# Kernel tuning notes

Hardware: AMD Instinct MI355X
Metric: run time of the kernel (lower is better)

## Reference

```python
import jax, jax.numpy as jnp
import numpy as np

D_MODEL = 1024
NUM_HEADS = 16
D_K = D_MODEL // NUM_HEADS
SCALE = 1.0 / (D_K ** 0.5)


def setup_inputs() -> dict:
    key = jax.random.key(0)
    k1, k2, k3 = jax.random.split(key, 3)
    x = jax.random.normal(k1, (2, 2048, D_MODEL), dtype=jnp.float32)
    # torch nn.Linear weight layout: [out_features, in_features]; y = x @ W.T
    w_qkv = jax.random.normal(k2, (3 * D_MODEL, D_MODEL), dtype=jnp.float32) * (1.0 / np.sqrt(D_MODEL))
    w_out = jax.random.normal(k3, (D_MODEL, D_MODEL), dtype=jnp.float32) * (1.0 / np.sqrt(D_MODEL))
    return {"x": x, "w_qkv": w_qkv, "w_out": w_out}


def reference(x, w_qkv, w_out):
    b, s, _ = x.shape
    qkv = jnp.einsum("bsd,ed->bse", x, w_qkv)            # [b, s, 3*d_model]
    q, k, v = jnp.split(qkv, 3, axis=-1)
    # [b, s, h, d_k] -> [b, h, s, d_k]
    q = q.reshape(b, s, NUM_HEADS, D_K).transpose(0, 2, 1, 3)
    k = k.reshape(b, s, NUM_HEADS, D_K).transpose(0, 2, 1, 3)
    v = v.reshape(b, s, NUM_HEADS, D_K).transpose(0, 2, 1, 3)
    scores = jnp.einsum("bhqd,bhkd->bhqk", q, k) * SCALE   # [b, h, s, s]
    attn = jax.nn.softmax(scores, axis=-1)
    ctx = jnp.einsum("bhqk,bhkd->bhqd", attn, v)           # [b, h, s, d_k]
    ctx = ctx.transpose(0, 2, 1, 3).reshape(b, s, D_MODEL)
    return jnp.einsum("bsd,ed->bse", ctx, w_out)
```

## Files before the change

kernel.cpp:

```cpp
#include <hip/hip_runtime.h>

typedef __attribute__((ext_vector_type(8))) short bf16x8;
typedef __attribute__((ext_vector_type(4))) float f32x4;
typedef __attribute__((ext_vector_type(16))) float f32x16;
typedef __attribute__((ext_vector_type(4))) unsigned int u32x4;

#define MFMA16(A, B, C) __builtin_amdgcn_mfma_f32_16x16x32_bf16((A), (B), (C), 0, 0, 0)
#define MFMA32(A, B, C) __builtin_amdgcn_mfma_f32_32x32x16_bf16((A), (B), (C), 0, 0, 0)

static __device__ __forceinline__ unsigned short f32_to_bf16(float f) {
    unsigned int u = __builtin_bit_cast(unsigned int, f);
    u += 0x7fffu + ((u >> 16) & 1u);
    return (unsigned short)(u >> 16);
}

static __device__ __forceinline__ unsigned int cvtpk(float lo, float hi) {
    unsigned int r;
    asm("v_cvt_pk_bf16_f32 %0, %1, %2" : "=v"(r) : "v"(lo), "v"(hi));
    return r;
}

static __device__ __forceinline__ void gload16(const unsigned short* g, unsigned short* l) {
    __builtin_amdgcn_global_load_lds(
        (const __attribute__((address_space(1))) unsigned int*)g,
        (__attribute__((address_space(3))) unsigned int*)l, 16, 0, 0);
}

#define QSCALE 0.18033688011112042f

__global__ void cast3_f32_bf16(const float* __restrict__ x, const float* __restrict__ wq,
                               const float* __restrict__ wo,
                               unsigned short* __restrict__ xb, unsigned short* __restrict__ wqb,
                               unsigned short* __restrict__ wob) {
    int i = blockIdx.x * 256 + threadIdx.x;
    const float* src;
    unsigned short* dst;
    int off;
    if (i < 1048576)      { src = x;  dst = xb;  off = i; }
    else if (i < 1835008) { src = wq; dst = wqb; off = i - 1048576; }
    else                  { src = wo; dst = wob; off = i - 1835008; }
    float4 v = reinterpret_cast<const float4*>(src)[off];
    ushort4 o;
    o.x = f32_to_bf16(v.x);
    o.y = f32_to_bf16(v.y);
    o.z = f32_to_bf16(v.z);
    o.w = f32_to_bf16(v.w);
    reinterpret_cast<ushort4*>(dst)[off] = o;
}

template <int MODE, int BM, int BN, int WR, int WC>
__global__ __launch_bounds__(256, 2)
void gemm_bt(const unsigned short* __restrict__ Ag,
             const unsigned short* __restrict__ Bg,
             int N, int K,
             unsigned short* __restrict__ qO,
             unsigned short* __restrict__ kO,
             unsigned short* __restrict__ vO,
             float* __restrict__ fO)
{
    constexpr int BK = 64;
    constexpr int MFR = BM / WR / 16;
    constexpr int NFR = BN / WC / 16;
    __shared__ unsigned short SMEM[(BM + BN) * BK];
    unsigned short* sA = SMEM;
    unsigned short* sB = SMEM + BM * BK;

    const int m0 = blockIdx.y * BM;
    const int n0 = blockIdx.x * BN;
    const int t = threadIdx.x;
    const int lane = t & 63;
    const int wid = t >> 6;
    const int wr = wid / WC, wc = wid % WC;
    const int g = lane >> 4, r = lane & 15;
    const int lr8 = lane >> 3, lc = lane & 7;

    const f32x4 fzero = {0.f, 0.f, 0.f, 0.f};
    f32x4 acc[MFR][NFR];
#pragma unroll
    for (int mi = 0; mi < MFR; ++mi)
#pragma unroll
        for (int ni = 0; ni < NFR; ++ni) acc[mi][ni] = fzero;

    for (int k0 = 0; k0 < K; k0 += BK) {
        __syncthreads();
#pragma unroll
        for (int rep = 0; rep < BM / 32; ++rep) {
            const int rbase = rep * 32 + wid * 8;
            const int row = rbase + lr8;
            const int cs = lc ^ (row & 7);
            gload16(&Ag[(size_t)(m0 + row) * K + k0 + cs * 8], &sA[rbase * 64]);
        }
#pragma unroll
        for (int rep = 0; rep < BN / 32; ++rep) {
            const int rbase = rep * 32 + wid * 8;
            const int row = rbase + lr8;
            const int cs = lc ^ (row & 7);
            gload16(&Bg[(size_t)(n0 + row) * K + k0 + cs * 8], &sB[rbase * 64]);
        }
        __syncthreads();

#pragma unroll
        for (int ks = 0; ks < BK; ks += 32) {
            const int c = (ks >> 3) + g;
            bf16x8 af[MFR], bfr[NFR];
#pragma unroll
            for (int mi = 0; mi < MFR; ++mi) {
                const int row = wr * (BM / WR) + mi * 16 + r;
                af[mi] = *reinterpret_cast<const bf16x8*>(&sA[row * BK + ((c * 8) ^ ((row & 7) * 8))]);
            }
#pragma unroll
            for (int ni = 0; ni < NFR; ++ni) {
                const int row = wc * (BN / WC) + ni * 16 + r;
                bfr[ni] = *reinterpret_cast<const bf16x8*>(&sB[row * BK + ((c * 8) ^ ((row & 7) * 8))]);
            }
#pragma unroll
            for (int mi = 0; mi < MFR; ++mi)
#pragma unroll
                for (int ni = 0; ni < NFR; ++ni)
                    acc[mi][ni] = MFMA16(af[mi], bfr[ni], acc[mi][ni]);
        }
    }

    if (MODE == 0) {
        const int which = n0 >> 10;
        if (which == 2) {
#pragma unroll
            for (int mi = 0; mi < MFR; ++mi) {
#pragma unroll
                for (int ni = 0; ni < NFR; ++ni) {
                    const int mbase = m0 + wr * (BM / WR) + mi * 16 + 4 * g;
                    const int n = n0 + wc * (BN / WC) + ni * 16 + r;
                    const int b = mbase >> 11, s = mbase & 2047;
                    const int h = (n >> 6) & 15;
                    const int d = n & 63;
                    ushort4 v4;
                    v4.x = f32_to_bf16(acc[mi][ni][0]);
                    v4.y = f32_to_bf16(acc[mi][ni][1]);
                    v4.z = f32_to_bf16(acc[mi][ni][2]);
                    v4.w = f32_to_bf16(acc[mi][ni][3]);
                    *reinterpret_cast<ushort4*>(&vO[(((size_t)(b * 16 + h)) * 64 + d) * 2048 + s]) = v4;
                }
            }
        } else {
            __syncthreads();
            unsigned short* T = &SMEM[wid * 4096];
            const float scl = (which == 0) ? QSCALE : 1.0f;
#pragma unroll
            for (int mi = 0; mi < MFR; ++mi) {
#pragma unroll
                for (int ni = 0; ni < NFR; ++ni) {
#pragma unroll
                    for (int i = 0; i < 4; ++i) {
                        const int m_l = mi * 16 + 4 * g + i;
                        const int n_l = ni * 16 + r;
                        const int pos = m_l * 64 + ((((n_l >> 3) ^ (m_l & 7)) << 3) | (n_l & 7));
                        T[pos] = f32_to_bf16(acc[mi][ni][i] * scl);
                    }
                }
            }
            const int b = (m0 + wr * 64) >> 11;
            const int sbase = (m0 + wr * 64) & 2047;
            const int hh = ((n0 + wc * 64) >> 6) & 15;
            unsigned short* qk = (which == 0) ? qO : kO;
            const size_t base = (((size_t)(b * 16 + hh)) * 2048 + sbase) * 64;
#pragma unroll
            for (int it = 0; it < 8; ++it) {
                const int row = it * 8 + lr8;
                bf16x8 v8 = *reinterpret_cast<const bf16x8*>(&T[row * 64 + ((lc ^ (row & 7)) << 3)]);
                *reinterpret_cast<bf16x8*>(&qk[base + (size_t)row * 64 + lc * 8]) = v8;
            }
        }
    } else {
#pragma unroll
        for (int mi = 0; mi < MFR; ++mi) {
#pragma unroll
            for (int ni = 0; ni < NFR; ++ni) {
                const int mbase = m0 + wr * (BM / WR) + mi * 16 + 4 * g;
                const int n = n0 + wc * (BN / WC) + ni * 16 + r;
#pragma unroll
                for (int i = 0; i < 4; ++i)
                    fO[(size_t)(mbase + i) * N + n] = acc[mi][ni][i];
            }
        }
    }
}

__global__ __launch_bounds__(512, 4)
void attn_kernel(const unsigned short* __restrict__ Q,
                 const unsigned short* __restrict__ Kg,
                 const unsigned short* __restrict__ Vtg,
                 unsigned short* __restrict__ ctx)
{
    const int S = 2048;
    const int bid = blockIdx.x;
    const int swz = (bid & 7) * 64 + (bid >> 3);
    const int hb = swz >> 4;
    const int qb = swz & 15;
    const unsigned short* Qh = Q + (size_t)hb * S * 64;
    const unsigned short* Kh = Kg + (size_t)hb * S * 64;
    const unsigned short* Vh = Vtg + (size_t)hb * 64 * S;

    const int t = threadIdx.x, lane = t & 63, wid = t >> 6;
    const int half = wid >> 2, wq = wid & 3;
    const int l31 = lane & 31, lhi = lane >> 5;
    const int lr8 = lane >> 3, lc = lane & 7;
    const int q0 = qb * 128 + wq * 32;
    const int kbase = half * 1024;

    const int krow = (l31 & 19) | ((l31 & 4) << 1) | ((l31 & 8) >> 1);
    const int ksw = (krow & 7) ^ ((krow >> 3) & 3);
    const int vsw = (l31 & 7) ^ ((l31 >> 3) & 3);

    __shared__ unsigned short smem[2][2][2][64 * 64];

    bf16x8 qf[4];
#pragma unroll
    for (int dstep = 0; dstep < 4; ++dstep)
        qf[dstep] = *reinterpret_cast<const bf16x8*>(
            &Qh[(size_t)(q0 + l31) * 64 + dstep * 16 + lhi * 8]);

    f32x16 acc[2];
#pragma unroll
    for (int dt = 0; dt < 2; ++dt)
#pragma unroll
        for (int i = 0; i < 16; ++i) acc[dt][i] = 0.f;
    float lrun = 0.f;

#define STAGE(buf, k0)                                                                       \
    {                                                                                        \
        _Pragma("unroll")                                                                    \
        for (int rep = 0; rep < 2; ++rep) {                                                  \
            const int rbase = wq * 16 + rep * 8;                                             \
            const int row = rbase + lr8;                                                     \
            const int cs = lc ^ ((row & 7) ^ ((row >> 3) & 3));                              \
            gload16(&Kh[(size_t)((k0) + row) * 64 + cs * 8], &smem[half][buf][0][rbase * 64]); \
            gload16(&Vh[(size_t)row * S + (k0) + cs * 8], &smem[half][buf][1][rbase * 64]);  \
        }                                                                                    \
    }

    STAGE(0, kbase);

    for (int it = 0; it < 16; ++it) {
        __syncthreads();
        const int cur = it & 1;
        if (it < 15) {
            const int kn = kbase + (it + 1) * 64;
            if (cur) STAGE(0, kn) else STAGE(1, kn);
        }
        const unsigned short* kb = smem[half][cur][0];
        const unsigned short* vb = smem[half][cur][1];

        f32x16 st0, st1;
#pragma unroll
        for (int i = 0; i < 16; ++i) { st0[i] = 0.f; st1[i] = 0.f; }
        __builtin_amdgcn_s_setprio(1);
#pragma unroll
        for (int dstep = 0; dstep < 4; ++dstep) {
            const int c = dstep * 2 + lhi;
            bf16x8 kf0 = *reinterpret_cast<const bf16x8*>(&kb[krow * 64 + ((c ^ ksw) * 8)]);
            bf16x8 kf1 = *reinterpret_cast<const bf16x8*>(&kb[(32 + krow) * 64 + ((c ^ ksw) * 8)]);
            st0 = MFMA32(kf0, qf[dstep], st0);
            st1 = MFMA32(kf1, qf[dstep], st1);
        }
        __builtin_amdgcn_s_setprio(0);

#pragma unroll
        for (int i = 0; i < 16; ++i) {
            st0[i] = __builtin_amdgcn_exp2f(st0[i]);
            st1[i] = __builtin_amdgcn_exp2f(st1[i]);
        }
        float s8[8];
#pragma unroll
        for (int j = 0; j < 8; ++j)
            s8[j] = (st0[j] + st0[j + 8]) + (st1[j] + st1[j + 8]);
        lrun += ((s8[0] + s8[1]) + (s8[2] + s8[3])) + ((s8[4] + s8[5]) + (s8[6] + s8[7]));

        bf16x8 pf[4];
#define PACK8(stv, base, out)                                                  \
        {                                                                      \
            u32x4 wv;                                                          \
            wv[0] = cvtpk(stv[(base) + 0], stv[(base) + 1]);                   \
            wv[1] = cvtpk(stv[(base) + 2], stv[(base) + 3]);                   \
            wv[2] = cvtpk(stv[(base) + 4], stv[(base) + 5]);                   \
            wv[3] = cvtpk(stv[(base) + 6], stv[(base) + 7]);                   \
            out = __builtin_bit_cast(bf16x8, wv);                              \
        }
        PACK8(st0, 0, pf[0])
        PACK8(st0, 8, pf[1])
        PACK8(st1, 0, pf[2])
        PACK8(st1, 8, pf[3])
#undef PACK8

        __builtin_amdgcn_s_setprio(1);
#pragma unroll
        for (int dt = 0; dt < 2; ++dt) {
            const int rowd = dt * 32 + l31;
#pragma unroll
            for (int ks = 0; ks < 4; ++ks) {
                const int c = ks * 2 + lhi;
                bf16x8 vf = *reinterpret_cast<const bf16x8*>(&vb[rowd * 64 + ((c ^ vsw) * 8)]);
                acc[dt] = MFMA32(vf, pf[ks], acc[dt]);
            }
        }
        __builtin_amdgcn_s_setprio(0);
    }
#undef STAGE

    lrun += __shfl_xor(lrun, 32);

    __syncthreads();
    float* cb = reinterpret_cast<float*>(&smem[0][0][0][0]);
    if (half == 1) {
        float* base = cb + wq * 2112;
#pragma unroll
        for (int dt = 0; dt < 2; ++dt)
#pragma unroll
            for (int i = 0; i < 16; ++i)
                base[(dt * 16 + i) * 64 + lane] = acc[dt][i];
        if (lhi == 0) base[2048 + l31] = lrun;
    }
    __syncthreads();
    if (half == 0) {
        float* base = cb + wq * 2112;
        const float l1 = base[2048 + l31];
        const float rl = __builtin_amdgcn_rcpf(lrun + l1);
        const int b = hb >> 4, hh = hb & 15;
        const size_t rowbase = ((size_t)(b * 2048 + q0 + l31)) * 1024 + hh * 64;
#pragma unroll
        for (int dt = 0; dt < 2; ++dt) {
#pragma unroll
            for (int rg = 0; rg < 4; ++rg) {
                float v0 = (acc[dt][4 * rg + 0] + base[(dt * 16 + 4 * rg + 0) * 64 + lane]) * rl;
                float v1 = (acc[dt][4 * rg + 1] + base[(dt * 16 + 4 * rg + 1) * 64 + lane]) * rl;
                float v2 = (acc[dt][4 * rg + 2] + base[(dt * 16 + 4 * rg + 2) * 64 + lane]) * rl;
                float v3 = (acc[dt][4 * rg + 3] + base[(dt * 16 + 4 * rg + 3) * 64 + lane]) * rl;
                uint2 o;
                o.x = cvtpk(v0, v1);
                o.y = cvtpk(v2, v3);
                const int dbase = dt * 32 + rg * 8 + lhi * 4;
                *reinterpret_cast<uint2*>(&ctx[rowbase + dbase]) = o;
            }
        }
    }
}

extern "C" void kernel_launch(void* const* d_in, const int* in_sizes, int n_in,
                              void* d_out, int out_size, void* d_ws, size_t ws_size,
                              hipStream_t stream) {
    const float* x     = (const float*)d_in[0];
    const float* w_qkv = (const float*)d_in[1];
    const float* w_out = (const float*)d_in[2];
    float* out = (float*)d_out;

    unsigned short* xb    = (unsigned short*)d_ws;
    unsigned short* wqkvb = xb + 4194304;
    unsigned short* woutb = wqkvb + 3145728;
    unsigned short* qB    = woutb + 1048576;
    unsigned short* kB    = qB + 4194304;
    unsigned short* vB    = kB + 4194304;
    unsigned short* ctxB  = vB + 4194304;

    cast3_f32_bf16<<<8192, 256, 0, stream>>>(x, w_qkv, w_out, xb, wqkvb, woutb);

    gemm_bt<0, 128, 128, 2, 2><<<dim3(24, 32), 256, 0, stream>>>(xb, wqkvb, 3072, 1024, qB, kB, vB, nullptr);

    attn_kernel<<<512, 512, 0, stream>>>(qB, kB, vB, ctxB);

    gemm_bt<1, 64, 128, 1, 4><<<dim3(8, 64), 256, 0, stream>>>(ctxB, woutb, 1024, 1024, nullptr, nullptr, nullptr, out);
}
```

Before: 102.7 us.

## Single-buffer attention K/V LDS tiles to double occupancy

Drops the double-buffered K/V shared-memory staging in the attention kernel so each block uses half the LDS, and raises the launch-bounds occupancy hint from 4 to 8 blocks per CU. The epilogue cross-half reduction is split into two passes over smaller LDS scratch to fit the reduced allocation. In exchange, each iteration now loads then waits with an extra barrier, so prefetch overlap inside a block is lost and must be recovered by running more concurrent blocks; the tighter register bound could also cause spills.

```diff
diff --git a/kernel.cpp b/kernel.cpp
--- a/kernel.cpp
+++ b/kernel.cpp
@@ -185,7 +185,7 @@
     }
 }
 
-__global__ __launch_bounds__(512, 4)
+__global__ __launch_bounds__(512, 8)
 void attn_kernel(const unsigned short* __restrict__ Q,
                  const unsigned short* __restrict__ Kg,
                  const unsigned short* __restrict__ Vtg,
@@ -211,7 +211,7 @@
     const int ksw = (krow & 7) ^ ((krow >> 3) & 3);
     const int vsw = (l31 & 7) ^ ((l31 >> 3) & 3);
 
-    __shared__ unsigned short smem[2][2][2][64 * 64];
+    __shared__ unsigned short smem[2][2][64 * 64];
 
     bf16x8 qf[4];
 #pragma unroll
@@ -226,29 +226,24 @@
         for (int i = 0; i < 16; ++i) acc[dt][i] = 0.f;
     float lrun = 0.f;
 
-#define STAGE(buf, k0)                                                                       \
+#define STAGE(k0)                                                                            \
     {                                                                                        \
         _Pragma("unroll")                                                                    \
         for (int rep = 0; rep < 2; ++rep) {                                                  \
             const int rbase = wq * 16 + rep * 8;                                             \
             const int row = rbase + lr8;                                                     \
             const int cs = lc ^ ((row & 7) ^ ((row >> 3) & 3));                              \
-            gload16(&Kh[(size_t)((k0) + row) * 64 + cs * 8], &smem[half][buf][0][rbase * 64]); \
-            gload16(&Vh[(size_t)row * S + (k0) + cs * 8], &smem[half][buf][1][rbase * 64]);  \
+            gload16(&Kh[(size_t)((k0) + row) * 64 + cs * 8], &smem[half][0][rbase * 64]);    \
+            gload16(&Vh[(size_t)row * S + (k0) + cs * 8], &smem[half][1][rbase * 64]);       \
         }                                                                                    \
     }
-
-    STAGE(0, kbase);
 
     for (int it = 0; it < 16; ++it) {
         __syncthreads();
-        const int cur = it & 1;
-        if (it < 15) {
-            const int kn = kbase + (it + 1) * 64;
-            if (cur) STAGE(0, kn) else STAGE(1, kn);
-        }
-        const unsigned short* kb = smem[half][cur][0];
-        const unsigned short* vb = smem[half][cur][1];
+        STAGE(kbase + it * 64);
+        __syncthreads();
+        const unsigned short* kb = smem[half][0];
+        const unsigned short* vb = smem[half][1];
 
         f32x16 st0, st1;
 #pragma unroll
@@ -309,37 +304,52 @@
     lrun += __shfl_xor(lrun, 32);
 
     __syncthreads();
-    float* cb = reinterpret_cast<float*>(&smem[0][0][0][0]);
+    float* cb = reinterpret_cast<float*>(&smem[0][0][0]);
+    float* base = cb + wq * 1056;
+    const int b = hb >> 4, hh = hb & 15;
+    const size_t rowbase = ((size_t)(b * 2048 + q0 + l31)) * 1024 + hh * 64;
+    float rl = 0.f;
+
     if (half == 1) {
-        float* base = cb + wq * 2112;
-#pragma unroll
-        for (int dt = 0; dt < 2; ++dt)
-#pragma unroll
-            for (int i = 0; i < 16; ++i)
-                base[(dt * 16 + i) * 64 + lane] = acc[dt][i];
-        if (lhi == 0) base[2048 + l31] = lrun;
+#pragma unroll
+        for (int i = 0; i < 16; ++i)
+            base[i * 64 + lane] = acc[0][i];
+        if (lhi == 0) base[1024 + l31] = lrun;
     }
     __syncthreads();
     if (half == 0) {
-        float* base = cb + wq * 2112;
-        const float l1 = base[2048 + l31];
-        const float rl = __builtin_amdgcn_rcpf(lrun + l1);
-        const int b = hb >> 4, hh = hb & 15;
-        const size_t rowbase = ((size_t)(b * 2048 + q0 + l31)) * 1024 + hh * 64;
-#pragma unroll
-        for (int dt = 0; dt < 2; ++dt) {
-#pragma unroll
-            for (int rg = 0; rg < 4; ++rg) {
-                float v0 = (acc[dt][4 * rg + 0] + base[(dt * 16 + 4 * rg + 0) * 64 + lane]) * rl;
-                float v1 = (acc[dt][4 * rg + 1] + base[(dt * 16 + 4 * rg + 1) * 64 + lane]) * rl;
-                float v2 = (acc[dt][4 * rg + 2] + base[(dt * 16 + 4 * rg + 2) * 64 + lane]) * rl;
-                float v3 = (acc[dt][4 * rg + 3] + base[(dt * 16 + 4 * rg + 3) * 64 + lane]) * rl;
-                uint2 o;
-                o.x = cvtpk(v0, v1);
-                o.y = cvtpk(v2, v3);
-                const int dbase = dt * 32 + rg * 8 + lhi * 4;
-                *reinterpret_cast<uint2*>(&ctx[rowbase + dbase]) = o;
-            }
+        const float l1 = base[1024 + l31];
+        rl = __builtin_amdgcn_rcpf(lrun + l1);
+#pragma unroll
+        for (int rg = 0; rg < 4; ++rg) {
+            float v0 = (acc[0][4 * rg + 0] + base[(4 * rg + 0) * 64 + lane]) * rl;
+            float v1 = (acc[0][4 * rg + 1] + base[(4 * rg + 1) * 64 + lane]) * rl;
+            float v2 = (acc[0][4 * rg + 2] + base[(4 * rg + 2) * 64 + lane]) * rl;
+            float v3 = (acc[0][4 * rg + 3] + base[(4 * rg + 3) * 64 + lane]) * rl;
+            uint2 o;
+            o.x = cvtpk(v0, v1);
+            o.y = cvtpk(v2, v3);
+            *reinterpret_cast<uint2*>(&ctx[rowbase + rg * 8 + lhi * 4]) = o;
+        }
+    }
+    __syncthreads();
+    if (half == 1) {
+#pragma unroll
+        for (int i = 0; i < 16; ++i)
+            base[i * 64 + lane] = acc[1][i];
+    }
+    __syncthreads();
+    if (half == 0) {
+#pragma unroll
+        for (int rg = 0; rg < 4; ++rg) {
+            float v0 = (acc[1][4 * rg + 0] + base[(4 * rg + 0) * 64 + lane]) * rl;
+            float v1 = (acc[1][4 * rg + 1] + base[(4 * rg + 1) * 64 + lane]) * rl;
+            float v2 = (acc[1][4 * rg + 2] + base[(4 * rg + 2) * 64 + lane]) * rl;
+            float v3 = (acc[1][4 * rg + 3] + base[(4 * rg + 3) * 64 + lane]) * rl;
+            uint2 o;
+            o.x = cvtpk(v0, v1);
+            o.y = cvtpk(v2, v3);
+            *reinterpret_cast<uint2*>(&ctx[rowbase + 32 + rg * 8 + lhi * 4]) = o;
         }
     }
 }
```

After: 239.4 us. 2.33x slower.

## Pre-shuffle K and V into MFMA fragment order and load directly from global

Applied to the files above, without the earlier changes.

The QKV projection epilogue now writes K and V in a per-head, per-64-key-tile layout that matches the MFMA operand fragment order. The attention kernel then reads K and V fragments straight from global memory as contiguous 16-byte per-lane loads. This removes the LDS staging, double buffering and per-iteration __syncthreads. The trade-off is losing the explicit prefetch overlap, so global/L2 latency now sits directly in the MFMA loop. It relies on the compiler and the number of resident waves to hide that latency.

```diff
diff --git a/kernel.cpp b/kernel.cpp
--- a/kernel.cpp
+++ b/kernel.cpp
@@ -123,22 +123,27 @@
 
     if (MODE == 0) {
         const int which = n0 >> 10;
+        const int sblk = m0 + wr * 64;
+        const int b = sblk >> 11;
+        const int kt = (sblk & 2047) >> 6;
+        const int hh = ((n0 & 1023) >> 6) + wc;
         if (which == 2) {
+            const size_t hbase = ((size_t)(b * 16 + hh)) * 131072 + (size_t)kt * 4096;
+            const int j0 = 4 * (g & 1);
+            const int lhi_s = g >> 1;
 #pragma unroll
             for (int mi = 0; mi < MFR; ++mi) {
 #pragma unroll
                 for (int ni = 0; ni < NFR; ++ni) {
-                    const int mbase = m0 + wr * (BM / WR) + mi * 16 + 4 * g;
-                    const int n = n0 + wc * (BN / WC) + ni * 16 + r;
-                    const int b = mbase >> 11, s = mbase & 2047;
-                    const int h = (n >> 6) & 15;
-                    const int d = n & 63;
+                    const int d = ni * 16 + r;
+                    const int dt = d >> 5, l31v = d & 31;
                     ushort4 v4;
                     v4.x = f32_to_bf16(acc[mi][ni][0]);
                     v4.y = f32_to_bf16(acc[mi][ni][1]);
                     v4.z = f32_to_bf16(acc[mi][ni][2]);
                     v4.w = f32_to_bf16(acc[mi][ni][3]);
-                    *reinterpret_cast<ushort4*>(&vO[(((size_t)(b * 16 + h)) * 64 + d) * 2048 + s]) = v4;
+                    *reinterpret_cast<ushort4*>(
+                        &vO[hbase + dt * 2048 + mi * 512 + (lhi_s * 32 + l31v) * 8 + j0]) = v4;
                 }
             }
         } else {
@@ -158,16 +163,26 @@
                     }
                 }
             }
-            const int b = (m0 + wr * 64) >> 11;
-            const int sbase = (m0 + wr * 64) & 2047;
-            const int hh = ((n0 + wc * 64) >> 6) & 15;
-            unsigned short* qk = (which == 0) ? qO : kO;
-            const size_t base = (((size_t)(b * 16 + hh)) * 2048 + sbase) * 64;
-#pragma unroll
-            for (int it = 0; it < 8; ++it) {
-                const int row = it * 8 + lr8;
-                bf16x8 v8 = *reinterpret_cast<const bf16x8*>(&T[row * 64 + ((lc ^ (row & 7)) << 3)]);
-                *reinterpret_cast<bf16x8*>(&qk[base + (size_t)row * 64 + lc * 8]) = v8;
+            if (which == 0) {
+                const size_t base = (((size_t)(b * 16 + hh)) * 2048 + (sblk & 2047)) * 64;
+#pragma unroll
+                for (int it = 0; it < 8; ++it) {
+                    const int row = it * 8 + lr8;
+                    bf16x8 v8 = *reinterpret_cast<const bf16x8*>(&T[row * 64 + ((lc ^ (row & 7)) << 3)]);
+                    *reinterpret_cast<bf16x8*>(&qO[base + (size_t)row * 64 + lc * 8]) = v8;
+                }
+            } else {
+                const size_t hbase = ((size_t)(b * 16 + hh)) * 131072 + (size_t)kt * 4096;
+                const int l31k = lane & 31, lhik = lane >> 5;
+                const int kpi = (l31k & 19) | ((l31k & 4) << 1) | ((l31k & 8) >> 1);
+#pragma unroll
+                for (int f = 0; f < 8; ++f) {
+                    const int blk = f >> 2, dstep = f & 3;
+                    const int m_l = blk * 32 + kpi;
+                    const int c = dstep * 2 + lhik;
+                    bf16x8 v8 = *reinterpret_cast<const bf16x8*>(&T[m_l * 64 + ((c ^ (m_l & 7)) << 3)]);
+                    *reinterpret_cast<bf16x8*>(&kO[hbase + blk * 2048 + dstep * 512 + (size_t)lane * 8]) = v8;
+                }
             }
         }
     } else {
@@ -187,8 +202,8 @@
 
 __global__ __launch_bounds__(512, 4)
 void attn_kernel(const unsigned short* __restrict__ Q,
-                 const unsigned short* __restrict__ Kg,
-                 const unsigned short* __restrict__ Vtg,
+                 const unsigned short* __restrict__ Kf,
+                 const unsigned short* __restrict__ Vf,
                  unsigned short* __restrict__ ctx)
 {
     const int S = 2048;
@@ -197,21 +212,15 @@
     const int hb = swz >> 4;
     const int qb = swz & 15;
     const unsigned short* Qh = Q + (size_t)hb * S * 64;
-    const unsigned short* Kh = Kg + (size_t)hb * S * 64;
-    const unsigned short* Vh = Vtg + (size_t)hb * 64 * S;
+    const unsigned short* Kh = Kf + (size_t)hb * 131072;
+    const unsigned short* Vh = Vf + (size_t)hb * 131072;
 
     const int t = threadIdx.x, lane = t & 63, wid = t >> 6;
     const int half = wid >> 2, wq = wid & 3;
     const int l31 = lane & 31, lhi = lane >> 5;
-    const int lr8 = lane >> 3, lc = lane & 7;
     const int q0 = qb * 128 + wq * 32;
-    const int kbase = half * 1024;
-
-    const int krow = (l31 & 19) | ((l31 & 4) << 1) | ((l31 & 8) >> 1);
-    const int ksw = (krow & 7) ^ ((krow >> 3) & 3);
-    const int vsw = (l31 & 7) ^ ((l31 >> 3) & 3);
-
-    __shared__ unsigned short smem[2][2][2][64 * 64];
+
+    __shared__ float cb[8448];
 
     bf16x8 qf[4];
 #pragma unroll
@@ -226,41 +235,28 @@
         for (int i = 0; i < 16; ++i) acc[dt][i] = 0.f;
     float lrun = 0.f;
 
-#define STAGE(buf, k0)                                                                       \
-    {                                                                                        \
-        _Pragma("unroll")                                                                    \
-        for (int rep = 0; rep < 2; ++rep) {                                                  \
-            const int rbase = wq * 16 + rep * 8;                                             \
-            const int row = rbase + lr8;                                                     \
-            const int cs = lc ^ ((row & 7) ^ ((row >> 3) & 3));                              \
-            gload16(&Kh[(size_t)((k0) + row) * 64 + cs * 8], &smem[half][buf][0][rbase * 64]); \
-            gload16(&Vh[(size_t)row * S + (k0) + cs * 8], &smem[half][buf][1][rbase * 64]);  \
-        }                                                                                    \
-    }
-
-    STAGE(0, kbase);
+    const unsigned short* kbase = Kh + (size_t)(half * 16) * 4096 + (size_t)lane * 8;
+    const unsigned short* vbase = Vh + (size_t)(half * 16) * 4096 + (size_t)lane * 8;
 
     for (int it = 0; it < 16; ++it) {
-        __syncthreads();
-        const int cur = it & 1;
-        if (it < 15) {
-            const int kn = kbase + (it + 1) * 64;
-            if (cur) STAGE(0, kn) else STAGE(1, kn);
-        }
-        const unsigned short* kb = smem[half][cur][0];
-        const unsigned short* vb = smem[half][cur][1];
+        const unsigned short* kp = kbase + (size_t)it * 4096;
+        const unsigned short* vp = vbase + (size_t)it * 4096;
+
+        bf16x8 kf0[4], kf1[4];
+#pragma unroll
+        for (int ds = 0; ds < 4; ++ds) {
+            kf0[ds] = *reinterpret_cast<const bf16x8*>(kp + ds * 512);
+            kf1[ds] = *reinterpret_cast<const bf16x8*>(kp + 2048 + ds * 512);
+        }
 
         f32x16 st0, st1;
 #pragma unroll
         for (int i = 0; i < 16; ++i) { st0[i] = 0.f; st1[i] = 0.f; }
         __builtin_amdgcn_s_setprio(1);
 #pragma unroll
-        for (int dstep = 0; dstep < 4; ++dstep) {
-            const int c = dstep * 2 + lhi;
-            bf16x8 kf0 = *reinterpret_cast<const bf16x8*>(&kb[krow * 64 + ((c ^ ksw) * 8)]);
-            bf16x8 kf1 = *reinterpret_cast<const bf16x8*>(&kb[(32 + krow) * 64 + ((c ^ ksw) * 8)]);
-            st0 = MFMA32(kf0, qf[dstep], st0);
-            st1 = MFMA32(kf1, qf[dstep], st1);
+        for (int ds = 0; ds < 4; ++ds) {
+            st0 = MFMA32(kf0[ds], qf[ds], st0);
+            st1 = MFMA32(kf1[ds], qf[ds], st1);
         }
         __builtin_amdgcn_s_setprio(0);
 
@@ -294,24 +290,19 @@
         __builtin_amdgcn_s_setprio(1);
 #pragma unroll
         for (int dt = 0; dt < 2; ++dt) {
-            const int rowd = dt * 32 + l31;
 #pragma unroll
             for (int ks = 0; ks < 4; ++ks) {
-                const int c = ks * 2 + lhi;
-                bf16x8 vf = *reinterpret_cast<const bf16x8*>(&vb[rowd * 64 + ((c ^ vsw) * 8)]);
+                bf16x8 vf = *reinterpret_cast<const bf16x8*>(vp + dt * 2048 + ks * 512);
                 acc[dt] = MFMA32(vf, pf[ks], acc[dt]);
             }
         }
         __builtin_amdgcn_s_setprio(0);
     }
-#undef STAGE
 
     lrun += __shfl_xor(lrun, 32);
 
-    __syncthreads();
-    float* cb = reinterpret_cast<float*>(&smem[0][0][0][0]);
+    float* base = cb + wq * 2112;
     if (half == 1) {
-        float* base = cb + wq * 2112;
 #pragma unroll
         for (int dt = 0; dt < 2; ++dt)
 #pragma unroll
@@ -321,7 +312,6 @@
     }
     __syncthreads();
     if (half == 0) {
-        float* base = cb + wq * 2112;
         const float l1 = base[2048 + l31];
         const float rl = __builtin_amdgcn_rcpf(lrun + l1);
         const int b = hb >> 4, hh = hb & 15;
```

Result: slower. 112.7 us (+9.8%).
